# Kernel tuning notes

Hardware: AMD Instinct MI355X
Metric: run time of the kernel (lower is better)

## Reference

```python
import jax, jax.numpy as jnp
import numpy as np

EMB = 256

def setup_inputs() -> dict:
    key = jax.random.key(0)
    ks = jax.random.split(key, 7)
    c = EMB
    x = jax.random.normal(ks[0], (4, c, 64, 64), dtype=jnp.float32)
    s = 1.0 / np.sqrt(c)
    Wq = jax.random.uniform(ks[1], (c, c), jnp.float32, -s, s)
    bq = jax.random.uniform(ks[2], (c,), jnp.float32, -s, s)
    Wk = jax.random.uniform(ks[3], (c, c), jnp.float32, -s, s)
    bk = jax.random.uniform(ks[4], (c,), jnp.float32, -s, s)
    Wv = jax.random.uniform(ks[5], (c, c), jnp.float32, -s, s)
    bv = jax.random.uniform(ks[6], (c,), jnp.float32, -s, s)
    return {"x": x, "Wq": Wq, "bq": bq, "Wk": Wk, "bk": bk, "Wv": Wv, "bv": bv}

def reference(x, Wq, bq, Wk, bk, Wv, bv):
    b, c, h, w = x.shape
    scale = jnp.sqrt(jnp.float32(c))
    # [b, n, c] tokens, n = h*w
    xt = x.reshape(b, c, h * w).transpose(0, 2, 1)
    q = jnp.einsum('bnc,dc->bnd', xt, Wq) + bq
    k = jnp.einsum('bnc,dc->bnd', xt, Wk) + bk
    v = jnp.einsum('bnc,dc->bnd', xt, Wv) + bv
    dist = jnp.einsum('bnd,bmd->bnm', q, k) / scale  # [b, n, n]
    dist = jax.nn.softmax(dist, axis=-1)
    mem = jnp.einsum('bnm,bmd->bnd', dist, v)  # [b, n, c]
    # Original: permute(0,1,2) is identity, then raw view(b,c,h,w) -> reshape
    return mem.reshape(b, c, h, w)
```

## Files before the change

kernel.cpp:

```cpp
#include <hip/hip_runtime.h>

typedef __attribute__((ext_vector_type(8))) short short8;
typedef __attribute__((ext_vector_type(4))) short short4_t;
typedef __attribute__((ext_vector_type(4))) float float4_t;
typedef __attribute__((ext_vector_type(16))) float float16_t;
typedef __attribute__((ext_vector_type(2))) int int2_t;

#define NTOK 4096
#define CDIM 256
#define BPB (NTOK * CDIM)
#define C1 0.0901684400555602f

__device__ inline float bf2f(short s) {
    return __uint_as_float(((unsigned)(unsigned short)s) << 16);
}
__device__ inline short f2bf(float f) {
    unsigned u = __float_as_uint(f);
    return (short)((u + 0x7fffu + ((u >> 16) & 1u)) >> 16);
}
__device__ inline int cvtpk_bf16(float lo, float hi) {
    int d;
    asm("v_cvt_pk_bf16_f32 %0, %1, %2" : "=v"(d) : "v"(lo), "v"(hi));
    return d;
}
__device__ inline void gl_lds16(const void* g, void* l) {
    __builtin_amdgcn_global_load_lds(
        (const __attribute__((address_space(1))) unsigned int*)g,
        (__attribute__((address_space(3))) unsigned int*)l, 16, 0, 0);
}

__global__ void sniff_dtype(const unsigned* __restrict__ x, int* __restrict__ flag) {
    __shared__ int cnt;
    if (threadIdx.x == 0) cnt = 0;
    __syncthreads();
    int local = 0;
    for (int i = threadIdx.x; i < 1024; i += 256) {
        unsigned e = (x[i] >> 7) & 0xffu;
        if (e >= 100u && e <= 140u) local++;
    }
    atomicAdd(&cnt, local);
    __syncthreads();
    if (threadIdx.x == 0) flag[0] = (cnt >= 512) ? 1 : 0;
}

__global__ __launch_bounds__(256) void wprep(
    const void* __restrict__ Wq, const void* __restrict__ Wk,
    const void* __restrict__ Wv, const int* __restrict__ flag,
    short* __restrict__ Wb)
{
    const int base = (blockIdx.x * 256 + threadIdx.x) * 8;
    const int wsel = base >> 16, off = base & 65535;
    const void* W = (wsel == 0) ? Wq : (wsel == 1) ? Wk : Wv;
    short8 v;
    if (flag[0]) {
        v = *(const short8*)((const short*)W + off);
    } else {
        const float* f = (const float*)W + off;
        float4 a = *(const float4*)f;
        float4 c4 = *(const float4*)(f + 4);
        v[0]=f2bf(a.x);  v[1]=f2bf(a.y);  v[2]=f2bf(a.z);  v[3]=f2bf(a.w);
        v[4]=f2bf(c4.x); v[5]=f2bf(c4.y); v[6]=f2bf(c4.z); v[7]=f2bf(c4.w);
    }
    *(short8*)(Wb + base) = v;
}

template <bool PIN>
__global__ __launch_bounds__(256, 4) void qkv8(
    const void* __restrict__ xv, const short* __restrict__ Wb,
    const void* __restrict__ bq, const void* __restrict__ bk,
    const void* __restrict__ bv,
    const int* __restrict__ flag, int b0,
    short* __restrict__ qbase, short* __restrict__ kbase,
    short* __restrict__ vtbase)
{
    int nt, bl, wsel;
    if (PIN) {
        const int bid = blockIdx.x;
        wsel = bid >> 8;
        const int rem = bid & 255;
        bl = rem & 3; nt = rem >> 2;
    } else { nt = blockIdx.x; wsel = blockIdx.y; bl = blockIdx.z; }
    const int b = b0 + bl;
    const int n0 = nt * 64;
    const int tid = threadIdx.x;
    const int w = tid >> 6, lane = tid & 63, l15 = lane & 15, qd = lane >> 4;
    const int isbf = flag[0];

    __shared__ short obuf[64 * 264];

    short8 af[8];
    {
        const int n = n0 + 16 * w + l15;
        if (isbf) {
            const short* xs = (const short*)xv + (size_t)b * (CDIM * NTOK) + n;
            #pragma unroll
            for (int s = 0; s < 8; ++s) {
                short8 v;
                #pragma unroll
                for (int e = 0; e < 8; ++e)
                    v[e] = xs[(s * 32 + qd * 8 + e) * NTOK];
                af[s] = v;
            }
        } else {
            const float* xf = (const float*)xv + (size_t)b * (CDIM * NTOK) + n;
            #pragma unroll
            for (int s = 0; s < 8; ++s) {
                short8 v;
                #pragma unroll
                for (int e = 0; e < 8; ++e)
                    v[e] = f2bf(xf[(s * 32 + qd * 8 + e) * NTOK]);
                af[s] = v;
            }
        }
    }

    const short* W = Wb + wsel * 65536;
    const void* bp = (wsel == 0) ? bq : (wsel == 1) ? bk : bv;

    short8 wv[8], wn[8];
    {
        const short* wr = W + l15 * 256 + qd * 8;
        #pragma unroll
        for (int s = 0; s < 8; ++s) wv[s] = *(const short8*)(wr + s * 32);
    }
    #pragma unroll 1
    for (int dg = 0; dg < 16; ++dg) {
        const int d = dg * 16 + l15;
        if (dg + 1 < 16) {
            const short* wr = W + (dg * 16 + 16 + l15) * 256 + qd * 8;
            #pragma unroll
            for (int s = 0; s < 8; ++s) wn[s] = *(const short8*)(wr + s * 32);
        }
        float4_t acc = {0.f, 0.f, 0.f, 0.f};
        #pragma unroll
        for (int s = 0; s < 8; ++s)
            acc = __builtin_amdgcn_mfma_f32_16x16x32_bf16(af[s], wv[s], acc, 0, 0, 0);
        const float bias = isbf ? bf2f(((const short*)bp)[d])
                                : ((const float*)bp)[d];
        if (wsel < 2) {
            #pragma unroll
            for (int r = 0; r < 4; ++r)
                obuf[(16 * w + 4 * qd + r) * 264 + d] = f2bf(acc[r] + bias);
        } else {
            #pragma unroll
            for (int r = 0; r < 4; ++r)
                obuf[d * 66 + (16 * w + 4 * qd + r)] = f2bf(acc[r] + bias);
        }
        #pragma unroll
        for (int s = 0; s < 8; ++s) wv[s] = wn[s];
    }
    __syncthreads();

    if (wsel == 0) {
        short* qdst = qbase + (size_t)bl * BPB;
        const int rl = tid >> 2;
        #pragma unroll
        for (int u = 0; u < 8; ++u) {
            const int cc = (tid & 3) + 4 * u;
            short8 vv = *(const short8*)&obuf[rl * 264 + cc * 8];
            *(short8*)(qdst + (size_t)(n0 + rl) * 256 + cc * 8) = vv;
        }
    } else if (wsel == 1) {
        short* kdst = kbase + (size_t)bl * BPB;
        const int rl = tid >> 2;
        const int tile = (n0 + rl) >> 5, rit = rl & 31;
        #pragma unroll
        for (int u = 0; u < 8; ++u) {
            const int ccp = (tid & 3) + 4 * u;
            const int cc  = ccp ^ rit;
            short8 vv = *(const short8*)&obuf[rl * 264 + cc * 8];
            *(short8*)(kdst + (size_t)tile * 8192 + rit * 256 + ccp * 8) = vv;
        }
    } else {
        short* vtdst = vtbase + (size_t)bl * BPB;
        const int d = tid;
        #pragma unroll
        for (int u = 0; u < 8; ++u) {
            short8 vv = *(const short8*)&obuf[d * 66 + u * 8];
            const int tile = (n0 >> 5) + (u >> 2), ck = u & 3;
            const int pos = ((d & 1) * 4 + ck) ^ ((d >> 1) & 7);
            *(short8*)(vtdst + (size_t)tile * 8192 + (d >> 1) * 64 + pos * 8) = vv;
        }
    }
}

__global__ __launch_bounds__(256, 2) void flash13(
    const short* __restrict__ qb, const short* __restrict__ kb,
    const short* __restrict__ vtb,
    float* __restrict__ pO, float* __restrict__ pl)
{
    const int bid = blockIdx.x;
    const int bl = bid & 3, half = (bid >> 2) & 3, qt = bid >> 4;
    const int q0 = qt * 128;
    const int tid = threadIdx.x;
    const int w = tid >> 6, lane = tid & 63, l31 = lane & 31, h = lane >> 5;

    __shared__ __align__(16) char smem[65536];
    short* kbufA = (short*)smem;
    short* vbufA = (short*)(smem + 32768);

    const short* Q  = qb  + (size_t)bl * BPB;
    const char*  Kc = (const char*)(kb  + (size_t)bl * BPB);
    const char*  Vc = (const char*)(vtb + (size_t)bl * BPB);

    short8 qf[16];
    {
        const short* qrow = Q + (size_t)(q0 + 32 * w + l31) * 256 + h * 8;
        #pragma unroll
        for (int s = 0; s < 16; ++s)
            qf[s] = *(const short8*)(qrow + s * 16);
    }

    float16_t oacc[8];
    #pragma unroll
    for (int dt = 0; dt < 8; ++dt)
        #pragma unroll
        for (int r = 0; r < 16; ++r) oacc[dt][r] = 0.f;
    float ll0 = 0.f, ll1 = 0.f, ll2 = 0.f, ll3 = 0.f;

    const int KT0 = half * 32, KT1 = KT0 + 32;

    {
        const char* ks = Kc + ((size_t)KT0 << 14);
        const char* vs = Vc + ((size_t)KT0 << 14);
        char* kd = smem + tid * 16;
        char* vd = smem + 32768 + tid * 16;
        #pragma unroll
        for (int u = 0; u < 4; ++u) {
            gl_lds16(ks + u * 4096 + tid * 16, kd + u * 4096);
            gl_lds16(vs + u * 4096 + tid * 16, vd + u * 4096);
        }
    }

    float16_t se, so;
    #pragma unroll
    for (int r = 0; r < 16; ++r) { se[r] = 0.f; so[r] = 0.f; }
    short8 pa0, pa1;

    #pragma unroll 1
    for (int kt = KT0; kt < KT1; ++kt) {
        if (kt > KT0) {
            #pragma unroll
            for (int r = 0; r < 16; ++r) se[r] = exp2f((se[r] + so[r]) * C1);
            #pragma unroll
            for (int g = 0; g < 4; ++g) {
                ll0 += se[4 * g + 0]; ll1 += se[4 * g + 1];
                ll2 += se[4 * g + 2]; ll3 += se[4 * g + 3];
            }
            {
                int x0 = cvtpk_bf16(se[0], se[1]);
                int y0 = cvtpk_bf16(se[4], se[5]);
                int z0 = cvtpk_bf16(se[2], se[3]);
                int u0 = cvtpk_bf16(se[6], se[7]);
                int2_t r1 = __builtin_amdgcn_permlane32_swap(x0, y0, false, false);
                int2_t r2 = __builtin_amdgcn_permlane32_swap(z0, u0, false, false);
                union { int i[4]; short8 s8; } uu;
                uu.i[0] = r1[0]; uu.i[1] = r2[0]; uu.i[2] = r1[1]; uu.i[3] = r2[1];
                pa0 = uu.s8;
                int x1 = cvtpk_bf16(se[8],  se[9]);
                int y1 = cvtpk_bf16(se[12], se[13]);
                int z1 = cvtpk_bf16(se[10], se[11]);
                int u1 = cvtpk_bf16(se[14], se[15]);
                int2_t r3 = __builtin_amdgcn_permlane32_swap(x1, y1, false, false);
                int2_t r4 = __builtin_amdgcn_permlane32_swap(z1, u1, false, false);
                union { int i[4]; short8 s8; } vv;
                vv.i[0] = r3[0]; vv.i[1] = r4[0]; vv.i[2] = r3[1]; vv.i[3] = r4[1];
                pa1 = vv.s8;
            }
            {
                const short* vprev = vbufA + ((kt + 1) & 1) * 8192;
                __builtin_amdgcn_s_setprio(1);
                #pragma unroll
                for (int dt = 0; dt < 8; ++dt) {
                    const int d = 32 * dt + l31, d2 = d >> 1;
                    {
                        const int pos = (((d & 1) * 4 + h) ^ (d2 & 7));
                        short8 vf = *(const short8*)&vprev[d2 * 64 + pos * 8];
                        oacc[dt] = __builtin_amdgcn_mfma_f32_32x32x16_bf16(pa0, vf, oacc[dt], 0, 0, 0);
                    }
                    {
                        const int pos = (((d & 1) * 4 + 2 + h) ^ (d2 & 7));
                        short8 vf = *(const short8*)&vprev[d2 * 64 + pos * 8];
                        oacc[dt] = __builtin_amdgcn_mfma_f32_32x32x16_bf16(pa1, vf, oacc[dt], 0, 0, 0);
                    }
                }
                __builtin_amdgcn_s_setprio(0);
            }
        }

        asm volatile("s_waitcnt vmcnt(0) lgkmcnt(0)" ::: "memory");
        __builtin_amdgcn_sched_barrier(0);
        __builtin_amdgcn_s_barrier();
        __builtin_amdgcn_sched_barrier(0);

        if (kt + 1 < KT1) {
            const int alt = (kt + 1) & 1;
            const char* ks = Kc + ((size_t)(kt + 1) << 14);
            const char* vs = Vc + ((size_t)(kt + 1) << 14);
            char* kd = smem + alt * 16384 + tid * 16;
            char* vd = smem + 32768 + alt * 16384 + tid * 16;
            #pragma unroll
            for (int u = 0; u < 4; ++u) {
                gl_lds16(ks + u * 4096 + tid * 16, kd + u * 4096);
                gl_lds16(vs + u * 4096 + tid * 16, vd + u * 4096);
            }
        }

        {
            const short* kcur = kbufA + (kt & 1) * 8192;
            #pragma unroll
            for (int r = 0; r < 16; ++r) { se[r] = 0.f; so[r] = 0.f; }
            __builtin_amdgcn_s_setprio(1);
            #pragma unroll
            for (int j = 0; j < 8; ++j) {
                short8 ka = *(const short8*)
                    &kcur[l31 * 256 + (((4 * j + h) ^ l31) * 8)];
                se = __builtin_amdgcn_mfma_f32_32x32x16_bf16(ka, qf[2 * j], se, 0, 0, 0);
                short8 kb2 = *(const short8*)
                    &kcur[l31 * 256 + (((4 * j + 2 + h) ^ l31) * 8)];
                so = __builtin_amdgcn_mfma_f32_32x32x16_bf16(kb2, qf[2 * j + 1], so, 0, 0, 0);
            }
            __builtin_amdgcn_s_setprio(0);
        }
    }

    {
        #pragma unroll
        for (int r = 0; r < 16; ++r) se[r] = exp2f((se[r] + so[r]) * C1);
        #pragma unroll
        for (int g = 0; g < 4; ++g) {
            ll0 += se[4 * g + 0]; ll1 += se[4 * g + 1];
            ll2 += se[4 * g + 2]; ll3 += se[4 * g + 3];
        }
        int x0 = cvtpk_bf16(se[0], se[1]);
        int y0 = cvtpk_bf16(se[4], se[5]);
        int z0 = cvtpk_bf16(se[2], se[3]);
        int u0 = cvtpk_bf16(se[6], se[7]);
        int2_t r1 = __builtin_amdgcn_permlane32_swap(x0, y0, false, false);
        int2_t r2 = __builtin_amdgcn_permlane32_swap(z0, u0, false, false);
        union { int i[4]; short8 s8; } uu;
        uu.i[0] = r1[0]; uu.i[1] = r2[0]; uu.i[2] = r1[1]; uu.i[3] = r2[1];
        pa0 = uu.s8;
        int x1 = cvtpk_bf16(se[8],  se[9]);
        int y1 = cvtpk_bf16(se[12], se[13]);
        int z1 = cvtpk_bf16(se[10], se[11]);
        int u1 = cvtpk_bf16(se[14], se[15]);
        int2_t r3 = __builtin_amdgcn_permlane32_swap(x1, y1, false, false);
        int2_t r4 = __builtin_amdgcn_permlane32_swap(z1, u1, false, false);
        union { int i[4]; short8 s8; } vv;
        vv.i[0] = r3[0]; vv.i[1] = r4[0]; vv.i[2] = r3[1]; vv.i[3] = r4[1];
        pa1 = vv.s8;

        const short* vlast = vbufA + ((KT1 - 1) & 1) * 8192;
        #pragma unroll
        for (int dt = 0; dt < 8; ++dt) {
            const int d = 32 * dt + l31, d2 = d >> 1;
            {
                const int pos = (((d & 1) * 4 + h) ^ (d2 & 7));
                short8 vf = *(const short8*)&vlast[d2 * 64 + pos * 8];
                oacc[dt] = __builtin_amdgcn_mfma_f32_32x32x16_bf16(pa0, vf, oacc[dt], 0, 0, 0);
            }
            {
                const int pos = (((d & 1) * 4 + 2 + h) ^ (d2 & 7));
                short8 vf = *(const short8*)&vlast[d2 * 64 + pos * 8];
                oacc[dt] = __builtin_amdgcn_mfma_f32_32x32x16_bf16(pa1, vf, oacc[dt], 0, 0, 0);
            }
        }
    }

    const size_t idx = (size_t)(bl * 32 + qt) * 4 + half;
    {
        float v2 = (ll0 + ll1) + (ll2 + ll3);
        v2 += __shfl_xor(v2, 32, 64);
        if (h == 0) pl[idx * 128 + 32 * w + l31] = v2;
    }
    float* po = pO + idx * 32768;
    #pragma unroll
    for (int dt = 0; dt < 8; ++dt) {
        #pragma unroll
        for (int r = 0; r < 16; ++r) {
            const int qrow = 32 * w + (r & 3) + 8 * (r >> 2) + 4 * h;
            po[qrow * 256 + 32 * dt + l31] = oacc[dt][r];
        }
    }
}

__global__ __launch_bounds__(256) void combine4(
    const float* __restrict__ pO, const float* __restrict__ pl,
    const int* __restrict__ flag, void* __restrict__ outv)
{
    const int tid = threadIdx.x, w = tid >> 6, lane = tid & 63;
    const int isbf = flag[0];
    #pragma unroll 1
    for (int st = 0; st < 16; ++st) {
        const int row = blockIdx.x * 64 + st * 4 + w;
        const int bl = row >> 12, n = row & 4095;
        const int qt = n >> 7, prow = n & 127;
        const size_t bidx = (size_t)(bl * 32 + qt) * 4;
        const float* P0 = pO + bidx * 32768 + prow * 256 + lane * 4;
        float4 a = *(const float4*)P0;
        float4 b = *(const float4*)(P0 + 32768);
        float4 c = *(const float4*)(P0 + 65536);
        float4 d = *(const float4*)(P0 + 98304);
        const float inv = 1.0f /
            (pl[(bidx + 0) * 128 + prow] + pl[(bidx + 1) * 128 + prow] +
             pl[(bidx + 2) * 128 + prow] + pl[(bidx + 3) * 128 + prow]);
        float4 r;
        r.x = (a.x + b.x + c.x + d.x) * inv;
        r.y = (a.y + b.y + c.y + d.y) * inv;
        r.z = (a.z + b.z + c.z + d.z) * inv;
        r.w = (a.w + b.w + c.w + d.w) * inv;
        const size_t o = (size_t)row * 256 + lane * 4;
        if (isbf) {
            short4_t pk;
            pk[0] = f2bf(r.x); pk[1] = f2bf(r.y);
            pk[2] = f2bf(r.z); pk[3] = f2bf(r.w);
            *(short4_t*)((short*)outv + o) = pk;
        } else {
            *(float4*)((float*)outv + o) = r;
        }
    }
}

template <bool PIN, bool SPLIT>
__global__ __launch_bounds__(256, 2) void flash12(
    int b0, const short* __restrict__ qb, const short* __restrict__ kb,
    const short* __restrict__ vtb, const int* __restrict__ flag,
    void* __restrict__ outv, float* __restrict__ pO, float* __restrict__ pl)
{
    int qt, bl, half;
    if (SPLIT) {
        const int bid = blockIdx.x;
        bl = (bid >> 1) & 3; half = bid & 1; qt = bid >> 3;
    } else if (PIN) {
        bl = blockIdx.x & 3; qt = blockIdx.x >> 2; half = 0;
    } else { qt = blockIdx.x; bl = blockIdx.z; half = 0; }

    const int b = b0 + bl;
    const int q0 = qt * 64;
    const int tid = threadIdx.x;
    const int w = tid >> 6, lane = tid & 63, l31 = lane & 31, h = lane >> 5;
    const int wi = w & 1, wh = w >> 1;

    __shared__ __align__(16) char smem[67584];
    short* kbufA = (short*)smem;
    short* vbufA = (short*)(smem + 32768);
    float* lbuf  = (float*)(smem + 66560);

    const short* Q  = qb  + (size_t)bl * BPB;
    const char*  Kc = (const char*)(kb  + (size_t)bl * BPB);
    const char*  Vc = (const char*)(vtb + (size_t)bl * BPB);

    short8 qf[16];
    {
        const short* qrow = Q + (size_t)(q0 + 32 * wh + l31) * 256 + h * 8;
        #pragma unroll
        for (int s = 0; s < 16; ++s)
            qf[s] = *(const short8*)(qrow + s * 16);
    }

    float16_t oacc[4];
    #pragma unroll
    for (int dt = 0; dt < 4; ++dt)
        #pragma unroll
        for (int r = 0; r < 16; ++r) oacc[dt][r] = 0.f;
    float ll0 = 0.f, ll1 = 0.f, ll2 = 0.f, ll3 = 0.f;

    const int KT0 = SPLIT ? half * 64 : 0;
    const int KT1 = KT0 + (SPLIT ? 64 : 128);

    {
        const char* ks = Kc + ((size_t)KT0 << 14);
        const char* vs = Vc + ((size_t)KT0 << 14);
        char* kd = smem + tid * 16;
        char* vd = smem + 32768 + tid * 16;
        #pragma unroll
        for (int u = 0; u < 4; ++u) {
            gl_lds16(ks + u * 4096 + tid * 16, kd + u * 4096);
            gl_lds16(vs + u * 4096 + tid * 16, vd + u * 4096);
        }
    }
    __syncthreads();

    short8 pa0 = {0,0,0,0,0,0,0,0}, pa1 = {0,0,0,0,0,0,0,0};

    #pragma unroll 1
    for (int kt = KT0; kt < KT1; ++kt) {
        short* kcur  = kbufA + (kt & 1) * 8192;
        short* vprev = vbufA + ((kt + 1) & 1) * 8192;

        if (kt + 1 < KT1) {
            const char* ks = Kc + ((size_t)(kt + 1) << 14);
            char* kd = smem + (((kt + 1) & 1) << 14) + tid * 16;
            #pragma unroll
            for (int u = 0; u < 4; ++u)
                gl_lds16(ks + u * 4096 + tid * 16, kd + u * 4096);
        }

        float16_t se, so;
        #pragma unroll
        for (int r = 0; r < 16; ++r) { se[r] = 0.f; so[r] = 0.f; }
        #pragma unroll
        for (int j = 0; j < 8; ++j) {
            short8 ka = *(const short8*)
                &kcur[l31 * 256 + (((4 * j + h) ^ l31) * 8)];
            se = __builtin_amdgcn_mfma_f32_32x32x16_bf16(ka, qf[2 * j], se, 0, 0, 0);
            short8 kb2 = *(const short8*)
                &kcur[l31 * 256 + (((4 * j + 2 + h) ^ l31) * 8)];
            so = __builtin_amdgcn_mfma_f32_32x32x16_bf16(kb2, qf[2 * j + 1], so, 0, 0, 0);
        }

        if (kt > KT0) {
            #pragma unroll
            for (int dt = 0; dt < 4; ++dt) {
                const int d = 128 * wi + 32 * dt + l31, d2 = d >> 1;
                {
                    const int pos = (((d & 1) * 4 + h) ^ (d2 & 7));
                    short8 vf = *(const short8*)&vprev[d2 * 64 + pos * 8];
                    oacc[dt] = __builtin_amdgcn_mfma_f32_32x32x16_bf16(pa0, vf, oacc[dt], 0, 0, 0);
                }
                {
                    const int pos = (((d & 1) * 4 + 2 + h) ^ (d2 & 7));
                    short8 vf = *(const short8*)&vprev[d2 * 64 + pos * 8];
                    oacc[dt] = __builtin_amdgcn_mfma_f32_32x32x16_bf16(pa1, vf, oacc[dt], 0, 0, 0);
                }
            }
        }

        asm volatile("s_waitcnt lgkmcnt(0)" ::: "memory");
        __builtin_amdgcn_sched_barrier(0);
        __builtin_amdgcn_s_barrier();
        __builtin_amdgcn_sched_barrier(0);

        if (kt + 1 < KT1) {
            const char* vs = Vc + ((size_t)(kt + 1) << 14);
            char* vd = smem + 32768 + (((kt + 1) & 1) << 14) + tid * 16;
            #pragma unroll
            for (int u = 0; u < 4; ++u)
                gl_lds16(vs + u * 4096 + tid * 16, vd + u * 4096);
        }

        float pf[16];
        #pragma unroll
        for (int r = 0; r < 16; ++r) pf[r] = exp2f((se[r] + so[r]) * C1);
        #pragma unroll
        for (int g = 0; g < 4; ++g) {
            ll0 += pf[4 * g + 0]; ll1 += pf[4 * g + 1];
            ll2 += pf[4 * g + 2]; ll3 += pf[4 * g + 3];
        }
        {
            int x0 = cvtpk_bf16(pf[0], pf[1]);
            int y0 = cvtpk_bf16(pf[4], pf[5]);
            int z0 = cvtpk_bf16(pf[2], pf[3]);
            int u0 = cvtpk_bf16(pf[6], pf[7]);
            int2_t r1 = __builtin_amdgcn_permlane32_swap(x0, y0, false, false);
            int2_t r2 = __builtin_amdgcn_permlane32_swap(z0, u0, false, false);
            union { int i[4]; short8 s8; } uu;
            uu.i[0] = r1[0]; uu.i[1] = r2[0]; uu.i[2] = r1[1]; uu.i[3] = r2[1];
            pa0 = uu.s8;
            int x1 = cvtpk_bf16(pf[8],  pf[9]);
            int y1 = cvtpk_bf16(pf[12], pf[13]);
            int z1 = cvtpk_bf16(pf[10], pf[11]);
            int u1 = cvtpk_bf16(pf[14], pf[15]);
            int2_t r3 = __builtin_amdgcn_permlane32_swap(x1, y1, false, false);
            int2_t r4 = __builtin_amdgcn_permlane32_swap(z1, u1, false, false);
            union { int i[4]; short8 s8; } vv;
            vv.i[0] = r3[0]; vv.i[1] = r4[0]; vv.i[2] = r3[1]; vv.i[3] = r4[1];
            pa1 = vv.s8;
        }

        __syncthreads();
    }

    {
        short* vlast = vbufA + 8192;
        #pragma unroll
        for (int dt = 0; dt < 4; ++dt) {
            const int d = 128 * wi + 32 * dt + l31, d2 = d >> 1;
            {
                const int pos = (((d & 1) * 4 + h) ^ (d2 & 7));
                short8 vf = *(const short8*)&vlast[d2 * 64 + pos * 8];
                oacc[dt] = __builtin_amdgcn_mfma_f32_32x32x16_bf16(pa0, vf, oacc[dt], 0, 0, 0);
            }
            {
                const int pos = (((d & 1) * 4 + 2 + h) ^ (d2 & 7));
                short8 vf = *(const short8*)&vlast[d2 * 64 + pos * 8];
                oacc[dt] = __builtin_amdgcn_mfma_f32_32x32x16_bf16(pa1, vf, oacc[dt], 0, 0, 0);
            }
        }
    }

    {
        float v2 = (ll0 + ll1) + (ll2 + ll3);
        v2 += __shfl_xor(v2, 32, 64);
        if (h == 0 && wi == 0) lbuf[32 * wh + l31] = v2;
    }

    if (SPLIT) {
        const size_t pidx = (size_t)(bl * 64 + qt) * 2 + half;
        float* po = pO + pidx * 16384;
        #pragma unroll
        for (int dt = 0; dt < 4; ++dt) {
            const int dim = 128 * wi + 32 * dt + l31;
            #pragma unroll
            for (int r = 0; r < 16; ++r) {
                const int qrow = 32 * wh + (r & 3) + 8 * (r >> 2) + 4 * h;
                po[qrow * 256 + dim] = oacc[dt][r];
            }
        }
        __syncthreads();
        if (tid < 64) pl[pidx * 64 + tid] = lbuf[tid];
    } else {
        __syncthreads();
        float* obuf = (float*)smem;
        #pragma unroll
        for (int dt = 0; dt < 4; ++dt) {
            const int dim = 128 * wi + 32 * dt + l31;
            #pragma unroll
            for (int r = 0; r < 16; ++r) {
                const int qrow = 32 * wh + (r & 3) + 8 * (r >> 2) + 4 * h;
                obuf[qrow * 260 + dim] = oacc[dt][r];
            }
        }
        __syncthreads();
        {
            const int row = tid >> 2, q4 = (tid & 3) * 64;
            const float inv = 1.0f / lbuf[row];
            const float* src = obuf + row * 260 + q4;
            const size_t o = (size_t)(b * NTOK + q0 + row) * 256 + q4;
            if (flag[0]) {
                short* op = (short*)outv;
                #pragma unroll
                for (int g = 0; g < 4; ++g) {
                    float4 a  = *(const float4*)(src + g * 8);
                    float4 c4 = *(const float4*)(src + g * 8 + 4);
                    short8 pk;
                    pk[0]=f2bf(a.x*inv);  pk[1]=f2bf(a.y*inv);
                    pk[2]=f2bf(a.z*inv);  pk[3]=f2bf(a.w*inv);
                    pk[4]=f2bf(c4.x*inv); pk[5]=f2bf(c4.y*inv);
                    pk[6]=f2bf(c4.z*inv); pk[7]=f2bf(c4.w*inv);
                    *(short8*)(op + o + g * 8) = pk;
                }
            } else {
                float* op = (float*)outv;
                #pragma unroll
                for (int g = 0; g < 16; ++g) {
                    float4 a = *(const float4*)(src + g * 4);
                    a.x *= inv; a.y *= inv; a.z *= inv; a.w *= inv;
                    *(float4*)(op + o + g * 4) = a;
                }
            }
        }
    }
}

__global__ __launch_bounds__(256) void combine2(
    const float* __restrict__ pO, const float* __restrict__ pl,
    const int* __restrict__ flag, void* __restrict__ outv)
{
    const int tile = blockIdx.x, tid = threadIdx.x;
    const int row = tid >> 2, seg = (tid & 3) * 64;
    const float* A = pO + (size_t)tile * 32768 + row * 256 + seg;
    const float* B = A + 16384;
    const float inv = 1.0f / (pl[tile * 128 + row] + pl[tile * 128 + 64 + row]);
    const size_t o = ((size_t)tile * 64 + row) * 256 + seg;
    if (flag[0]) {
        short* op = (short*)outv;
        #pragma unroll
        for (int g = 0; g < 8; ++g) {
            float4 a  = *(const float4*)(A + g * 8);
            float4 a2 = *(const float4*)(A + g * 8 + 4);
            float4 c  = *(const float4*)(B + g * 8);
            float4 c2 = *(const float4*)(B + g * 8 + 4);
            short8 pk;
            pk[0]=f2bf((a.x+c.x)*inv);   pk[1]=f2bf((a.y+c.y)*inv);
            pk[2]=f2bf((a.z+c.z)*inv);   pk[3]=f2bf((a.w+c.w)*inv);
            pk[4]=f2bf((a2.x+c2.x)*inv); pk[5]=f2bf((a2.y+c2.y)*inv);
            pk[6]=f2bf((a2.z+c2.z)*inv); pk[7]=f2bf((a2.w+c2.w)*inv);
            *(short8*)(op + o + g * 8) = pk;
        }
    } else {
        float* op = (float*)outv;
        #pragma unroll
        for (int g = 0; g < 16; ++g) {
            float4 a = *(const float4*)(A + g * 4);
            float4 c = *(const float4*)(B + g * 4);
            a.x = (a.x + c.x) * inv; a.y = (a.y + c.y) * inv;
            a.z = (a.z + c.z) * inv; a.w = (a.w + c.w) * inv;
            *(float4*)(op + o + g * 4) = a;
        }
    }
}

extern "C" void kernel_launch(void* const* d_in, const int* in_sizes, int n_in,
                              void* d_out, int out_size, void* d_ws, size_t ws_size,
                              hipStream_t stream)
{
    const size_t HDR = 256;
    const size_t WBB = 393216;
    const size_t TB  = (size_t)BPB * 2;
    const size_t OFF_K = HDR + WBB;
    const size_t need_prim = OFF_K + 12 * TB;
    const size_t PO2 = 33554432;
    const size_t need_s2 = need_prim + PO2 + 131072;
    const size_t PO4 = 67108864;
    const size_t need_s4 = need_prim + PO4 + 262144;

    int*   flag = (int*)d_ws;
    short* Wb   = (short*)((char*)d_ws + HDR);

    sniff_dtype<<<1, 256, 0, stream>>>((const unsigned*)d_in[0], flag);
    wprep<<<96, 256, 0, stream>>>(d_in[1], d_in[3], d_in[5], flag, Wb);

    if (ws_size >= need_prim) {
        short* kbase  = (short*)((char*)d_ws + OFF_K);
        short* vtbase = kbase  + 4 * (size_t)BPB;
        short* qbase  = vtbase + 4 * (size_t)BPB;
        qkv8<true><<<dim3(768, 1, 1), 256, 0, stream>>>(
            d_in[0], Wb, d_in[2], d_in[4], d_in[6], flag, 0,
            qbase, kbase, vtbase);
        if (ws_size >= need_s4) {
            float* pO = (float*)((char*)d_ws + need_prim);
            float* pl = (float*)((char*)d_ws + need_prim + PO4);
            flash13<<<dim3(512, 1, 1), 256, 0, stream>>>(
                qbase, kbase, vtbase, pO, pl);
            combine4<<<dim3(256, 1, 1), 256, 0, stream>>>(pO, pl, flag, d_out);
        } else if (ws_size >= need_s2) {
            float* pO = (float*)((char*)d_ws + need_prim);
            float* pl = (float*)((char*)d_ws + need_prim + PO2);
            flash12<true, true><<<dim3(512, 1, 1), 256, 0, stream>>>(
                0, qbase, kbase, vtbase, flag, d_out, pO, pl);
            combine2<<<dim3(256, 1, 1), 256, 0, stream>>>(pO, pl, flag, d_out);
        } else {
            flash12<true, false><<<dim3(256, 1, 1), 256, 0, stream>>>(
                0, qbase, kbase, vtbase, flag, d_out, nullptr, nullptr);
        }
        return;
    }

    int nb = 4;
    while (nb > 1 && ws_size < OFF_K + (size_t)nb * 3 * TB) nb--;
    short* kbase  = (short*)((char*)d_ws + OFF_K);
    short* vtbase = kbase + (size_t)nb * BPB;
    short* qbase  = vtbase + (size_t)nb * BPB;

    for (int b0 = 0; b0 < 4; b0 += nb) {
        const int nbc = (4 - b0) < nb ? (4 - b0) : nb;
        qkv8<false><<<dim3(64, 3, nbc), 256, 0, stream>>>(
            d_in[0], Wb, d_in[2], d_in[4], d_in[6], flag, b0,
            qbase, kbase, vtbase);
        flash12<false, false><<<dim3(64, 1, nbc), 256, 0, stream>>>(
            b0, qbase, kbase, vtbase, flag, d_out, nullptr, nullptr);
    }
}
```

Before: 224.7 us.

## Pre-transpose x into token-major bf16 before QKV projection, drop setprio

Adds an xprep kernel that converts x to bf16 and transposes it through shared memory into a token-major buffer, so the QKV kernel loads A fragments with contiguous 16-byte loads instead of strided scalar gathers. Previously x was read three times, once per projection. The QKV kernel also stops double-buffering W fragments and loads them each iteration, and the flash kernel drops its s_setprio hints. This costs an extra launch and an extra round trip of x through global memory, and changes the workspace layout so xt aliases the partial-output buffer.

```diff
diff --git a/kernel.cpp b/kernel.cpp
--- a/kernel.cpp
+++ b/kernel.cpp
@@ -65,11 +65,57 @@
 }
 
 template <bool PIN>
-__global__ __launch_bounds__(256, 4) void qkv8(
-    const void* __restrict__ xv, const short* __restrict__ Wb,
+__global__ __launch_bounds__(256, 3) void xprep(
+    const void* __restrict__ xv, const int* __restrict__ flag,
+    short* __restrict__ xt, int b0)
+{
+    int nt, bl;
+    if (PIN) { bl = blockIdx.x & 3; nt = blockIdx.x >> 2; }
+    else     { nt = blockIdx.x; bl = blockIdx.z; }
+    const int b = b0 + bl;
+    const int n0 = nt * 64;
+    const int tid = threadIdx.x;
+    const int isbf = flag[0];
+
+    __shared__ short ls[64 * 264];
+
+    {
+        const size_t xb = (size_t)b * (CDIM * NTOK) + (size_t)tid * NTOK + n0;
+        if (isbf) {
+            const short* x = (const short*)xv + xb;
+            #pragma unroll
+            for (int i = 0; i < 8; ++i) {
+                short8 v = *(const short8*)(x + i * 8);
+                #pragma unroll
+                for (int j = 0; j < 8; ++j) ls[(i * 8 + j) * 264 + tid] = v[j];
+            }
+        } else {
+            const float* x = (const float*)xv + xb;
+            #pragma unroll
+            for (int i = 0; i < 16; ++i) {
+                float4 v = *(const float4*)(x + i * 4);
+                ls[(i * 4 + 0) * 264 + tid] = f2bf(v.x);
+                ls[(i * 4 + 1) * 264 + tid] = f2bf(v.y);
+                ls[(i * 4 + 2) * 264 + tid] = f2bf(v.z);
+                ls[(i * 4 + 3) * 264 + tid] = f2bf(v.w);
+            }
+        }
+    }
+    __syncthreads();
+
+    const int rl = tid >> 2, c0 = (tid & 3) * 64;
+    short* dst = xt + (size_t)bl * BPB + (size_t)(n0 + rl) * 256 + c0;
+    #pragma unroll
+    for (int u = 0; u < 8; ++u)
+        *(short8*)(dst + u * 8) = *(const short8*)&ls[rl * 264 + c0 + u * 8];
+}
+
+template <bool PIN>
+__global__ __launch_bounds__(256, 4) void qkv9(
+    const short* __restrict__ xt, const short* __restrict__ Wb,
     const void* __restrict__ bq, const void* __restrict__ bk,
     const void* __restrict__ bv,
-    const int* __restrict__ flag, int b0,
+    const int* __restrict__ flag,
     short* __restrict__ qbase, short* __restrict__ kbase,
     short* __restrict__ vtbase)
 {
@@ -80,7 +126,6 @@
         const int rem = bid & 255;
         bl = rem & 3; nt = rem >> 2;
     } else { nt = blockIdx.x; wsel = blockIdx.y; bl = blockIdx.z; }
-    const int b = b0 + bl;
     const int n0 = nt * 64;
     const int tid = threadIdx.x;
     const int w = tid >> 6, lane = tid & 63, l15 = lane & 15, qd = lane >> 4;
@@ -90,47 +135,23 @@
 
     short8 af[8];
     {
-        const int n = n0 + 16 * w + l15;
-        if (isbf) {
-            const short* xs = (const short*)xv + (size_t)b * (CDIM * NTOK) + n;
-            #pragma unroll
-            for (int s = 0; s < 8; ++s) {
-                short8 v;
-                #pragma unroll
-                for (int e = 0; e < 8; ++e)
-                    v[e] = xs[(s * 32 + qd * 8 + e) * NTOK];
-                af[s] = v;
-            }
-        } else {
-            const float* xf = (const float*)xv + (size_t)b * (CDIM * NTOK) + n;
-            #pragma unroll
-            for (int s = 0; s < 8; ++s) {
-                short8 v;
-                #pragma unroll
-                for (int e = 0; e < 8; ++e)
-                    v[e] = f2bf(xf[(s * 32 + qd * 8 + e) * NTOK]);
-                af[s] = v;
-            }
-        }
+        const short* xr = xt + (size_t)bl * BPB
+                        + (size_t)(n0 + 16 * w + l15) * 256 + qd * 8;
+        #pragma unroll
+        for (int s = 0; s < 8; ++s)
+            af[s] = *(const short8*)(xr + s * 32);
     }
 
     const short* W = Wb + wsel * 65536;
     const void* bp = (wsel == 0) ? bq : (wsel == 1) ? bk : bv;
 
-    short8 wv[8], wn[8];
-    {
-        const short* wr = W + l15 * 256 + qd * 8;
-        #pragma unroll
-        for (int s = 0; s < 8; ++s) wv[s] = *(const short8*)(wr + s * 32);
-    }
     #pragma unroll 1
     for (int dg = 0; dg < 16; ++dg) {
         const int d = dg * 16 + l15;
-        if (dg + 1 < 16) {
-            const short* wr = W + (dg * 16 + 16 + l15) * 256 + qd * 8;
-            #pragma unroll
-            for (int s = 0; s < 8; ++s) wn[s] = *(const short8*)(wr + s * 32);
-        }
+        const short* wr = W + d * 256 + qd * 8;
+        short8 wv[8];
+        #pragma unroll
+        for (int s = 0; s < 8; ++s) wv[s] = *(const short8*)(wr + s * 32);
         float4_t acc = {0.f, 0.f, 0.f, 0.f};
         #pragma unroll
         for (int s = 0; s < 8; ++s)
@@ -146,8 +167,6 @@
             for (int r = 0; r < 4; ++r)
                 obuf[d * 66 + (16 * w + 4 * qd + r)] = f2bf(acc[r] + bias);
         }
-        #pragma unroll
-        for (int s = 0; s < 8; ++s) wv[s] = wn[s];
     }
     __syncthreads();
 
@@ -269,7 +288,6 @@
             }
             {
                 const short* vprev = vbufA + ((kt + 1) & 1) * 8192;
-                __builtin_amdgcn_s_setprio(1);
                 #pragma unroll
                 for (int dt = 0; dt < 8; ++dt) {
                     const int d = 32 * dt + l31, d2 = d >> 1;
@@ -284,7 +302,6 @@
                         oacc[dt] = __builtin_amdgcn_mfma_f32_32x32x16_bf16(pa1, vf, oacc[dt], 0, 0, 0);
                     }
                 }
-                __builtin_amdgcn_s_setprio(0);
             }
         }
 
@@ -310,7 +327,6 @@
             const short* kcur = kbufA + (kt & 1) * 8192;
             #pragma unroll
             for (int r = 0; r < 16; ++r) { se[r] = 0.f; so[r] = 0.f; }
-            __builtin_amdgcn_s_setprio(1);
             #pragma unroll
             for (int j = 0; j < 8; ++j) {
                 short8 ka = *(const short8*)
@@ -320,7 +336,6 @@
                     &kcur[l31 * 256 + (((4 * j + 2 + h) ^ l31) * 8)];
                 so = __builtin_amdgcn_mfma_f32_32x32x16_bf16(kb2, qf[2 * j + 1], so, 0, 0, 0);
             }
-            __builtin_amdgcn_s_setprio(0);
         }
     }
 
@@ -699,6 +714,7 @@
     const size_t HDR = 256;
     const size_t WBB = 393216;
     const size_t TB  = (size_t)BPB * 2;
+    const size_t XTB = 4 * TB;
     const size_t OFF_K = HDR + WBB;
     const size_t need_prim = OFF_K + 12 * TB;
     const size_t PO2 = 33554432;
@@ -712,43 +728,55 @@
     sniff_dtype<<<1, 256, 0, stream>>>((const unsigned*)d_in[0], flag);
     wprep<<<96, 256, 0, stream>>>(d_in[1], d_in[3], d_in[5], flag, Wb);
 
-    if (ws_size >= need_prim) {
+    if (ws_size >= need_s2) {
         short* kbase  = (short*)((char*)d_ws + OFF_K);
         short* vtbase = kbase  + 4 * (size_t)BPB;
         short* qbase  = vtbase + 4 * (size_t)BPB;
-        qkv8<true><<<dim3(768, 1, 1), 256, 0, stream>>>(
-            d_in[0], Wb, d_in[2], d_in[4], d_in[6], flag, 0,
-            qbase, kbase, vtbase);
+        float* pO = (float*)((char*)d_ws + need_prim);
+        short* xt = (short*)pO;
+        xprep<true><<<dim3(256, 1, 1), 256, 0, stream>>>(d_in[0], flag, xt, 0);
+        qkv9<true><<<dim3(768, 1, 1), 256, 0, stream>>>(
+            xt, Wb, d_in[2], d_in[4], d_in[6], flag, qbase, kbase, vtbase);
         if (ws_size >= need_s4) {
-            float* pO = (float*)((char*)d_ws + need_prim);
             float* pl = (float*)((char*)d_ws + need_prim + PO4);
             flash13<<<dim3(512, 1, 1), 256, 0, stream>>>(
                 qbase, kbase, vtbase, pO, pl);
             combine4<<<dim3(256, 1, 1), 256, 0, stream>>>(pO, pl, flag, d_out);
-        } else if (ws_size >= need_s2) {
-            float* pO = (float*)((char*)d_ws + need_prim);
+        } else {
             float* pl = (float*)((char*)d_ws + need_prim + PO2);
             flash12<true, true><<<dim3(512, 1, 1), 256, 0, stream>>>(
                 0, qbase, kbase, vtbase, flag, d_out, pO, pl);
             combine2<<<dim3(256, 1, 1), 256, 0, stream>>>(pO, pl, flag, d_out);
-        } else {
-            flash12<true, false><<<dim3(256, 1, 1), 256, 0, stream>>>(
-                0, qbase, kbase, vtbase, flag, d_out, nullptr, nullptr);
         }
         return;
     }
 
+    if (ws_size >= need_prim + XTB) {
+        short* kbase  = (short*)((char*)d_ws + OFF_K);
+        short* vtbase = kbase  + 4 * (size_t)BPB;
+        short* qbase  = vtbase + 4 * (size_t)BPB;
+        short* xt     = qbase  + 4 * (size_t)BPB;
+        xprep<true><<<dim3(256, 1, 1), 256, 0, stream>>>(d_in[0], flag, xt, 0);
+        qkv9<true><<<dim3(768, 1, 1), 256, 0, stream>>>(
+            xt, Wb, d_in[2], d_in[4], d_in[6], flag, qbase, kbase, vtbase);
+        flash12<true, false><<<dim3(256, 1, 1), 256, 0, stream>>>(
+            0, qbase, kbase, vtbase, flag, d_out, nullptr, nullptr);
+        return;
+    }
+
     int nb = 4;
-    while (nb > 1 && ws_size < OFF_K + (size_t)nb * 3 * TB) nb--;
+    while (nb > 1 && ws_size < OFF_K + (size_t)nb * 4 * TB) nb--;
     short* kbase  = (short*)((char*)d_ws + OFF_K);
-    short* vtbase = kbase + (size_t)nb * BPB;
+    short* vtbase = kbase  + (size_t)nb * BPB;
     short* qbase  = vtbase + (size_t)nb * BPB;
+    short* xt     = qbase  + (size_t)nb * BPB;
 
     for (int b0 = 0; b0 < 4; b0 += nb) {
         const int nbc = (4 - b0) < nb ? (4 - b0) : nb;
-        qkv8<false><<<dim3(64, 3, nbc), 256, 0, stream>>>(
-            d_in[0], Wb, d_in[2], d_in[4], d_in[6], flag, b0,
-            qbase, kbase, vtbase);
+        xprep<false><<<dim3(64, 1, nbc), 256, 0, stream>>>(
+            d_in[0], flag, xt, b0);
+        qkv9<false><<<dim3(64, 3, nbc), 256, 0, stream>>>(
+            xt, Wb, d_in[2], d_in[4], d_in[6], flag, qbase, kbase, vtbase);
         flash12<false, false><<<dim3(64, 1, nbc), 256, 0, stream>>>(
             b0, qbase, kbase, vtbase, flag, d_out, nullptr, nullptr);
     }
```

Measured after the change: 237.3 us. +5.6%, slower.

## Fuse dtype sniff into weight prep and split-K combine into flash kernel

Applied to the files above, without the earlier changes.

Merges the dtype detection kernel into the weight-conversion kernel so every block computes the flag itself, and drops the separate combine launch. Instead, the last of the four split blocks per query tile, found with an atomic ticket counter, reduces the partial outputs and writes the final result. It also removes the s_setprio hints around the MFMA loops. This saves two kernel launches and their serialization gaps, at the cost of redundant sniff work per block, atomic and fence overhead, and a tail where only one block per tile does the combine.

```diff
diff --git a/kernel.cpp b/kernel.cpp
--- a/kernel.cpp
+++ b/kernel.cpp
@@ -29,30 +29,33 @@
         (__attribute__((address_space(3))) unsigned int*)l, 16, 0, 0);
 }
 
-__global__ void sniff_dtype(const unsigned* __restrict__ x, int* __restrict__ flag) {
-    __shared__ int cnt;
-    if (threadIdx.x == 0) cnt = 0;
+__global__ __launch_bounds__(256) void wprep2(
+    const void* __restrict__ Wq, const void* __restrict__ Wk,
+    const void* __restrict__ Wv, const unsigned* __restrict__ x,
+    int* __restrict__ flag, int* __restrict__ cnt, short* __restrict__ Wb)
+{
+    __shared__ int cs;
+    if (threadIdx.x == 0) cs = 0;
     __syncthreads();
     int local = 0;
     for (int i = threadIdx.x; i < 1024; i += 256) {
         unsigned e = (x[i] >> 7) & 0xffu;
         if (e >= 100u && e <= 140u) local++;
     }
-    atomicAdd(&cnt, local);
+    atomicAdd(&cs, local);
     __syncthreads();
-    if (threadIdx.x == 0) flag[0] = (cnt >= 512) ? 1 : 0;
-}
-
-__global__ __launch_bounds__(256) void wprep(
-    const void* __restrict__ Wq, const void* __restrict__ Wk,
-    const void* __restrict__ Wv, const int* __restrict__ flag,
-    short* __restrict__ Wb)
-{
+    const int isbf = (cs >= 512) ? 1 : 0;
+
+    if (blockIdx.x == 0) {
+        if (threadIdx.x == 0) flag[0] = isbf;
+        if (threadIdx.x < 128) cnt[threadIdx.x] = 0;
+    }
+
     const int base = (blockIdx.x * 256 + threadIdx.x) * 8;
     const int wsel = base >> 16, off = base & 65535;
     const void* W = (wsel == 0) ? Wq : (wsel == 1) ? Wk : Wv;
     short8 v;
-    if (flag[0]) {
+    if (isbf) {
         v = *(const short8*)((const short*)W + off);
     } else {
         const float* f = (const float*)W + off;
@@ -184,9 +187,10 @@
     }
 }
 
-__global__ __launch_bounds__(256, 2) void flash13(
+__global__ __launch_bounds__(256, 2) void flash13f(
     const short* __restrict__ qb, const short* __restrict__ kb,
-    const short* __restrict__ vtb,
+    const short* __restrict__ vtb, const int* __restrict__ flag,
+    int* __restrict__ cnt, void* __restrict__ outv,
     float* __restrict__ pO, float* __restrict__ pl)
 {
     const int bid = blockIdx.x;
@@ -196,6 +200,7 @@
     const int w = tid >> 6, lane = tid & 63, l31 = lane & 31, h = lane >> 5;
 
     __shared__ __align__(16) char smem[65536];
+    __shared__ int tkt;
     short* kbufA = (short*)smem;
     short* vbufA = (short*)(smem + 32768);
 
@@ -269,7 +274,6 @@
             }
             {
                 const short* vprev = vbufA + ((kt + 1) & 1) * 8192;
-                __builtin_amdgcn_s_setprio(1);
                 #pragma unroll
                 for (int dt = 0; dt < 8; ++dt) {
                     const int d = 32 * dt + l31, d2 = d >> 1;
@@ -284,7 +288,6 @@
                         oacc[dt] = __builtin_amdgcn_mfma_f32_32x32x16_bf16(pa1, vf, oacc[dt], 0, 0, 0);
                     }
                 }
-                __builtin_amdgcn_s_setprio(0);
             }
         }
 
@@ -310,7 +313,6 @@
             const short* kcur = kbufA + (kt & 1) * 8192;
             #pragma unroll
             for (int r = 0; r < 16; ++r) { se[r] = 0.f; so[r] = 0.f; }
-            __builtin_amdgcn_s_setprio(1);
             #pragma unroll
             for (int j = 0; j < 8; ++j) {
                 short8 ka = *(const short8*)
@@ -320,7 +322,6 @@
                     &kcur[l31 * 256 + (((4 * j + 2 + h) ^ l31) * 8)];
                 so = __builtin_amdgcn_mfma_f32_32x32x16_bf16(kb2, qf[2 * j + 1], so, 0, 0, 0);
             }
-            __builtin_amdgcn_s_setprio(0);
         }
     }
 
@@ -368,7 +369,8 @@
         }
     }
 
-    const size_t idx = (size_t)(bl * 32 + qt) * 4 + half;
+    const int tile = bl * 32 + qt;
+    const size_t idx = (size_t)tile * 4 + half;
     {
         float v2 = (ll0 + ll1) + (ll2 + ll3);
         v2 += __shfl_xor(v2, 32, 64);
@@ -383,41 +385,42 @@
             po[qrow * 256 + 32 * dt + l31] = oacc[dt][r];
         }
     }
-}
-
-__global__ __launch_bounds__(256) void combine4(
-    const float* __restrict__ pO, const float* __restrict__ pl,
-    const int* __restrict__ flag, void* __restrict__ outv)
-{
-    const int tid = threadIdx.x, w = tid >> 6, lane = tid & 63;
-    const int isbf = flag[0];
-    #pragma unroll 1
-    for (int st = 0; st < 16; ++st) {
-        const int row = blockIdx.x * 64 + st * 4 + w;
-        const int bl = row >> 12, n = row & 4095;
-        const int qt = n >> 7, prow = n & 127;
-        const size_t bidx = (size_t)(bl * 32 + qt) * 4;
-        const float* P0 = pO + bidx * 32768 + prow * 256 + lane * 4;
-        float4 a = *(const float4*)P0;
-        float4 b = *(const float4*)(P0 + 32768);
-        float4 c = *(const float4*)(P0 + 65536);
-        float4 d = *(const float4*)(P0 + 98304);
-        const float inv = 1.0f /
-            (pl[(bidx + 0) * 128 + prow] + pl[(bidx + 1) * 128 + prow] +
-             pl[(bidx + 2) * 128 + prow] + pl[(bidx + 3) * 128 + prow]);
-        float4 r;
-        r.x = (a.x + b.x + c.x + d.x) * inv;
-        r.y = (a.y + b.y + c.y + d.y) * inv;
-        r.z = (a.z + b.z + c.z + d.z) * inv;
-        r.w = (a.w + b.w + c.w + d.w) * inv;
-        const size_t o = (size_t)row * 256 + lane * 4;
-        if (isbf) {
-            short4_t pk;
-            pk[0] = f2bf(r.x); pk[1] = f2bf(r.y);
-            pk[2] = f2bf(r.z); pk[3] = f2bf(r.w);
-            *(short4_t*)((short*)outv + o) = pk;
-        } else {
-            *(float4*)((float*)outv + o) = r;
+
+    __syncthreads();
+    if (tid == 0) {
+        __threadfence();
+        tkt = atomicAdd(&cnt[tile], 1);
+    }
+    __syncthreads();
+    if (tkt == 3) {
+        __threadfence();
+        const int isbf = flag[0];
+        const float* pb  = pO + (size_t)tile * 4 * 32768;
+        const float* plb = pl + (size_t)tile * 4 * 128;
+        #pragma unroll 1
+        for (int rr = 0; rr < 32; ++rr) {
+            const int prow = w * 32 + rr;
+            const float inv = 1.0f / (plb[prow] + plb[128 + prow]
+                                    + plb[256 + prow] + plb[384 + prow]);
+            const float* p0 = pb + prow * 256 + lane * 4;
+            float4 a  = *(const float4*)p0;
+            float4 b2 = *(const float4*)(p0 + 32768);
+            float4 c  = *(const float4*)(p0 + 65536);
+            float4 d  = *(const float4*)(p0 + 98304);
+            float4 r;
+            r.x = (a.x + b2.x + c.x + d.x) * inv;
+            r.y = (a.y + b2.y + c.y + d.y) * inv;
+            r.z = (a.z + b2.z + c.z + d.z) * inv;
+            r.w = (a.w + b2.w + c.w + d.w) * inv;
+            const size_t o = (size_t)(bl * NTOK + q0 + prow) * 256 + lane * 4;
+            if (isbf) {
+                short4_t pk;
+                pk[0] = f2bf(r.x); pk[1] = f2bf(r.y);
+                pk[2] = f2bf(r.z); pk[3] = f2bf(r.w);
+                *(short4_t*)((short*)outv + o) = pk;
+            } else {
+                *(float4*)((float*)outv + o) = r;
+            }
         }
     }
 }
@@ -696,7 +699,7 @@
                               void* d_out, int out_size, void* d_ws, size_t ws_size,
                               hipStream_t stream)
 {
-    const size_t HDR = 256;
+    const size_t HDR = 1024;
     const size_t WBB = 393216;
     const size_t TB  = (size_t)BPB * 2;
     const size_t OFF_K = HDR + WBB;
@@ -707,10 +710,11 @@
     const size_t need_s4 = need_prim + PO4 + 262144;
 
     int*   flag = (int*)d_ws;
+    int*   cnt  = (int*)((char*)d_ws + 64);
     short* Wb   = (short*)((char*)d_ws + HDR);
 
-    sniff_dtype<<<1, 256, 0, stream>>>((const unsigned*)d_in[0], flag);
-    wprep<<<96, 256, 0, stream>>>(d_in[1], d_in[3], d_in[5], flag, Wb);
+    wprep2<<<96, 256, 0, stream>>>(
+        d_in[1], d_in[3], d_in[5], (const unsigned*)d_in[0], flag, cnt, Wb);
 
     if (ws_size >= need_prim) {
         short* kbase  = (short*)((char*)d_ws + OFF_K);
@@ -722,9 +726,8 @@
         if (ws_size >= need_s4) {
             float* pO = (float*)((char*)d_ws + need_prim);
             float* pl = (float*)((char*)d_ws + need_prim + PO4);
-            flash13<<<dim3(512, 1, 1), 256, 0, stream>>>(
-                qbase, kbase, vtbase, pO, pl);
-            combine4<<<dim3(256, 1, 1), 256, 0, stream>>>(pO, pl, flag, d_out);
+            flash13f<<<dim3(512, 1, 1), 256, 0, stream>>>(
+                qbase, kbase, vtbase, flag, cnt, d_out, pO, pl);
         } else if (ws_size >= need_s2) {
             float* pO = (float*)((char*)d_ws + need_prim);
             float* pl = (float*)((char*)d_ws + need_prim + PO2);
```

New measurement: 280.1 us. 1.25x slower.
